# Performance work log

Hardware: AMD Instinct MI355X
Metric: run time of the kernel (lower is better)

Reference implementation:

```python
import jax, jax.numpy as jnp
import numpy as np

H, C = 4, 32
NT, NDAT, NDEV = 50000, 20000, 4
EDT, EVT, ETT = 800000, 200000, 400000


def _gat_conv(xs, xd, src, dst, ea, Ws, Wd, We, As, Ad, Ae, b, n_dst, concat):
    # linear projections -> [N, H, C]
    hs = (xs @ Ws).reshape(-1, H, C)
    hd = (xd @ Wd).reshape(-1, H, C)
    he = (ea @ We).reshape(-1, H, C)
    # per-edge attention logits [E, H]
    al = (hs * As).sum(-1)[src] + (hd * Ad).sum(-1)[dst] + (he * Ae).sum(-1)
    al = jax.nn.leaky_relu(al, 0.2)
    # segment softmax over incoming edges of each dst node
    amax = jax.ops.segment_max(al, dst, num_segments=n_dst)
    amax = jnp.where(jnp.isfinite(amax), amax, 0.0)
    ex = jnp.exp(al - amax[dst])
    den = jax.ops.segment_sum(ex, dst, num_segments=n_dst)
    w = ex / (den[dst] + 1e-16)
    # weighted scatter-add of source messages
    out = jax.ops.segment_sum(hs[src] * w[..., None], dst, num_segments=n_dst)
    out = out.reshape(n_dst, H * C) if concat else out.mean(axis=1)
    return out + b


def _add_self_loops_mean(src, dst, ea, n):
    # PyG add_self_loops(fill_value='mean'): loop edge_attr = mean of incoming edge_attr per node
    cnt = jax.ops.segment_sum(jnp.ones(dst.shape, ea.dtype), dst, num_segments=n)
    ea_mean = jax.ops.segment_sum(ea, dst, num_segments=n) / jnp.maximum(cnt, 1.0)[:, None]
    loops = jnp.arange(n, dtype=src.dtype)
    return (jnp.concatenate([src, loops]), jnp.concatenate([dst, loops]),
            jnp.concatenate([ea, ea_mean], axis=0))


def setup_inputs() -> dict:
    key = jax.random.key(0)
    ks = iter(jax.random.split(key, 40))
    nrm = lambda shape, fan: jax.random.normal(next(ks), shape, jnp.float32) / np.sqrt(fan)
    inp = {}
    inp['x_data'] = jax.random.normal(next(ks), (NDAT, 8), jnp.float32)
    inp['x_tasks'] = jax.random.normal(next(ks), (NT, 16), jnp.float32)
    inp['x_dev'] = jax.random.normal(next(ks), (NDEV, 8), jnp.float32)
    inp['ei_dt'] = jnp.stack([jax.random.randint(next(ks), (EDT,), 0, NDAT),
                              jax.random.randint(next(ks), (EDT,), 0, NT)]).astype(jnp.int32)
    inp['ea_dt'] = jax.random.normal(next(ks), (EDT, 8), jnp.float32)
    inp['ei_vt'] = jnp.stack([jax.random.randint(next(ks), (EVT,), 0, NDEV),
                              jax.random.randint(next(ks), (EVT,), 0, NT)]).astype(jnp.int32)
    inp['ea_vt'] = jax.random.normal(next(ks), (EVT, 6), jnp.float32)
    inp['ei_tt'] = jnp.stack([jax.random.randint(next(ks), (ETT,), 0, NT),
                              jax.random.randint(next(ks), (ETT,), 0, NT)]).astype(jnp.int32)
    inp['ea_tt'] = jax.random.normal(next(ks), (ETT, 4), jnp.float32)
    # conv1: (data -> tasks), concat=True
    inp['Ws1'] = nrm((8, H * C), 8); inp['Wd1'] = nrm((16, H * C), 16); inp['We1'] = nrm((8, H * C), 8)
    inp['As1'] = nrm((H, C), C); inp['Ad1'] = nrm((H, C), C); inp['Ae1'] = nrm((H, C), C)
    inp['b1'] = jnp.zeros((H * C,), jnp.float32)
    # conv2: (devices -> tasks), concat=True
    inp['Ws2'] = nrm((8, H * C), 8); inp['Wd2'] = nrm((16, H * C), 16); inp['We2'] = nrm((6, H * C), 6)
    inp['As2'] = nrm((H, C), C); inp['Ad2'] = nrm((H, C), C); inp['Ae2'] = nrm((H, C), C)
    inp['b2'] = jnp.zeros((H * C,), jnp.float32)
    # conv3: tasks -> tasks, single lin (256 -> H*C), concat=False, self loops
    inp['W3'] = nrm((2 * H * C, H * C), 2 * H * C); inp['We3'] = nrm((4, H * C), 4)
    inp['As3'] = nrm((H, C), C); inp['Ad3'] = nrm((H, C), C); inp['Ae3'] = nrm((H, C), C)
    inp['b3'] = jnp.zeros((C,), jnp.float32)
    return inp


def reference(x_data, x_tasks, x_dev, ei_dt, ea_dt, ei_vt, ea_vt, ei_tt, ea_tt,
              Ws1, Wd1, We1, As1, Ad1, Ae1, b1,
              Ws2, Wd2, We2, As2, Ad2, Ae2, b2,
              W3, We3, As3, Ad3, Ae3, b3):
    t_data = jax.nn.relu(_gat_conv(x_data, x_tasks, ei_dt[0], ei_dt[1], ea_dt,
                                   Ws1, Wd1, We1, As1, Ad1, Ae1, b1, NT, True))
    t_dev = jax.nn.relu(_gat_conv(x_dev, x_tasks, ei_vt[0], ei_vt[1], ea_vt,
                                  Ws2, Wd2, We2, As2, Ad2, Ae2, b2, NT, True))
    tasks = jnp.concatenate([t_data, t_dev], axis=1)  # [NT, 256]
    src, dst, ea = _add_self_loops_mean(ei_tt[0], ei_tt[1], ea_tt, NT)
    x = _gat_conv(tasks, tasks, src, dst, ea, W3, W3, We3, As3, Ad3, Ae3, b3, NT, False)
    x = jax.nn.relu(x)
    # dropout(p=0.5) is identity in eval mode
    return x
```

## Files before the change

### kernel.cpp

```cpp
#include <hip/hip_runtime.h>
#include <math.h>

static const int NT = 50000, NDAT = 20000, NDEV = 4;
static const int EDT = 800000, EVT = 200000, ETT = 400000;

static const int SCAN_TILE = 2048, SCAN_NB = 25;

static const int IN_A = NDAT * 128;
static const int IN_B = IN_A + NDAT * 4;
static const int IN_C = IN_B + NT * 4;
static const int IN_D = IN_C + NDEV * 128;
static const int IN_E = IN_D + NDEV * 4;
static const int IN_F = IN_E + 256 * 128;

static const size_t OFF_TASKS = 0;
static const size_t OFF_HS    = 12800000;
static const size_t OFF_RANK  = OFF_HS;
static const size_t OFF_HSB1  = OFF_HS + 1400000;
static const size_t OFF_WV1   = OFF_HS + 2680000;
static const size_t OFF_WV2   = 19200000;
static const size_t OFF_ESRC1 = 20000000;
static const size_t OFF_ESRC2 = 20800000;
static const size_t OFF_PERM3 = 21200000;
static const size_t OFF_DEG   = 23200000;
static const size_t OFF_RP    = 23350000;
static const size_t OFF_AS1   = 23500004;
static const size_t OFF_AD1   = 23580004;
static const size_t OFF_AD2   = 23780004;
static const size_t OFF_HS2   = 23980004;
static const size_t OFF_AS2   = 23980516;
static const size_t OFF_QS1   = 23980532;
static const size_t OFF_QD1   = 23980564;
static const size_t OFF_P1    = 23980628;
static const size_t OFF_QS2   = 23980660;
static const size_t OFF_QD2   = 23980692;
static const size_t OFF_P2    = 23980756;
static const size_t OFF_P3    = 23980780;
static const size_t OFF_BSUM  = 23980796;
static const size_t OFF_W3HT  = 23980924;
static const size_t OFF_W3LT  = 23997308;
static const size_t WS_TOTAL  = 24013692;

typedef short v8s __attribute__((ext_vector_type(8)));
typedef float v4f __attribute__((ext_vector_type(4)));

__device__ __forceinline__ float lrelu(float a) { return a > 0.f ? a : 0.2f * a; }
__device__ __forceinline__ unsigned short f2bf(float x) {
    unsigned int u = __float_as_uint(x);
    return (unsigned short)((u + 0x7FFFu + ((u >> 16) & 1u)) >> 16);
}
__device__ __forceinline__ float bf2f(unsigned short h) {
    return __uint_as_float(((unsigned int)h) << 16);
}
__device__ __forceinline__ void cvt_split(const float4& A, const float4& B, v8s& hi, v8s& lo) {
    union { unsigned short u[8]; v8s v; } H, L;
    float f[8] = {A.x, A.y, A.z, A.w, B.x, B.y, B.z, B.w};
    #pragma unroll
    for (int i = 0; i < 8; ++i) {
        unsigned short h = f2bf(f[i]);
        H.u[i] = h;
        L.u[i] = f2bf(f[i] - bf2f(h));
    }
    hi = H.v; lo = L.v;
}

__global__ void k_proj_small(const float* Ws1, const float* As1,
                             const float* Wd1, const float* Ad1,
                             const float* We1, const float* Ae1,
                             const float* Ws2, const float* As2,
                             const float* Wd2, const float* Ad2,
                             const float* We2, const float* Ae2,
                             const float* We3, const float* Ae3,
                             float* Qs1, float* Qd1, float* P1,
                             float* Qs2, float* Qd2, float* P2, float* P3) {
    int t = threadIdx.x;
    const float *W, *A; float* O; int u;
    if      (t < 32)  { W = Ws1; A = As1; O = Qs1; u = t; }
    else if (t < 96)  { W = Wd1; A = Ad1; O = Qd1; u = t - 32; }
    else if (t < 128) { W = We1; A = Ae1; O = P1;  u = t - 96; }
    else if (t < 160) { W = Ws2; A = As2; O = Qs2; u = t - 128; }
    else if (t < 224) { W = Wd2; A = Ad2; O = Qd2; u = t - 160; }
    else if (t < 248) { W = We2; A = Ae2; O = P2;  u = t - 224; }
    else if (t < 264) { W = We3; A = Ae3; O = P3;  u = t - 248; }
    else return;
    int k = u >> 2, h = u & 3;
    float acc = 0.f;
    for (int c = 0; c < 32; ++c) acc += W[k * 128 + h * 32 + c] * A[h * 32 + c];
    O[k * 4 + h] = acc;
}

__global__ __launch_bounds__(256) void k_inputs(const float* __restrict__ x_data,
                                                const float* __restrict__ Ws1,
                                                unsigned short* __restrict__ hsb1,
                                                const float* __restrict__ Qs1,
                                                float* __restrict__ as1,
                                                const float* __restrict__ x_tasks,
                                                const float* __restrict__ Qd1,
                                                const float* __restrict__ Qd2,
                                                float* __restrict__ ad1, float* __restrict__ ad2,
                                                const float* __restrict__ x_dev,
                                                const float* __restrict__ Ws2,
                                                float* __restrict__ hs2,
                                                const float* __restrict__ Qs2,
                                                float* __restrict__ as2,
                                                const float* __restrict__ W3,
                                                unsigned short* __restrict__ w3hT,
                                                unsigned short* __restrict__ w3lT) {
    int idx = blockIdx.x * blockDim.x + threadIdx.x;
    if (idx < IN_A) {
        int n = idx >> 7, j = idx & 127;
        float acc = 0.f;
        #pragma unroll
        for (int k = 0; k < 8; ++k) acc += x_data[n * 8 + k] * Ws1[k * 128 + j];
        hsb1[idx] = f2bf(acc);
    } else if (idx < IN_B) {
        int i = idx - IN_A;
        int n = i >> 2, h = i & 3;
        float acc = 0.f;
        #pragma unroll
        for (int k = 0; k < 8; ++k) acc += x_data[n * 8 + k] * Qs1[k * 4 + h];
        as1[i] = acc;
    } else if (idx < IN_C) {
        int i = idx - IN_B;
        int n = i >> 2, h = i & 3;
        float a = 0.f, b = 0.f;
        #pragma unroll
        for (int k = 0; k < 16; ++k) {
            float v = x_tasks[n * 16 + k];
            a += v * Qd1[k * 4 + h];
            b += v * Qd2[k * 4 + h];
        }
        ad1[i] = a; ad2[i] = b;
    } else if (idx < IN_D) {
        int i = idx - IN_C;
        int n = i >> 7, j = i & 127;
        float acc = 0.f;
        #pragma unroll
        for (int k = 0; k < 8; ++k) acc += x_dev[n * 8 + k] * Ws2[k * 128 + j];
        hs2[i] = acc;
    } else if (idx < IN_E) {
        int i = idx - IN_D;
        int n = i >> 2, h = i & 3;
        float acc = 0.f;
        #pragma unroll
        for (int k = 0; k < 8; ++k) acc += x_dev[n * 8 + k] * Qs2[k * 4 + h];
        as2[i] = acc;
    } else if (idx < IN_F) {
        int i = idx - IN_E;
        int k = i >> 7, n = i & 127;
        float x = W3[i];
        unsigned short h = f2bf(x);
        w3hT[n * 256 + k] = h;
        w3lT[n * 256 + k] = f2bf(x - bf2f(h));
    }
}

__global__ void k_hist(const int* __restrict__ dt, const int* __restrict__ vt,
                       const int* __restrict__ tt, int* __restrict__ deg,
                       int* __restrict__ rank) {
    int e = blockIdx.x * blockDim.x + threadIdx.x;
    if (e < EDT) rank[e] = atomicAdd(&deg[dt[EDT + e]], 1);
    else if (e < EDT + EVT) rank[e] = atomicAdd(&deg[NT + vt[EVT + (e - EDT)]], 1);
    else if (e < EDT + EVT + ETT) rank[e] = atomicAdd(&deg[2 * NT + tt[ETT + (e - EDT - EVT)]], 1);
}

__global__ __launch_bounds__(256) void k_scan_part(const int* __restrict__ deg,
                                                   int* __restrict__ bsum) {
    int b = blockIdx.x;
    int g = b / SCAN_NB, t = b % SCAN_NB;
    int base = t * SCAN_TILE + threadIdx.x * 8;
    const int* dg = deg + (size_t)g * NT;
    int s = 0;
    if (base + 8 <= NT) {
        int4 a = *reinterpret_cast<const int4*>(dg + base);
        int4 c = *reinterpret_cast<const int4*>(dg + base + 4);
        s = a.x + a.y + a.z + a.w + c.x + c.y + c.z + c.w;
    } else {
        for (int i = 0; i < 8; ++i) if (base + i < NT) s += dg[base + i];
    }
    __shared__ int red[256];
    red[threadIdx.x] = s;
    __syncthreads();
    for (int off = 128; off > 0; off >>= 1) {
        if (threadIdx.x < off) red[threadIdx.x] += red[threadIdx.x + off];
        __syncthreads();
    }
    if (threadIdx.x == 0) bsum[b] = red[0];
}

__global__ void k_scan_bsum(int* __restrict__ bsum, int* __restrict__ rp) {
    int lane = threadIdx.x;
    for (int g = 0; g < 3; ++g) {
        int v = (lane < SCAN_NB) ? bsum[g * SCAN_NB + lane] : 0;
        int inc = v;
        #pragma unroll
        for (int off = 1; off < 32; off <<= 1) {
            int o = __shfl_up(inc, off, 32);
            if ((lane & 31) >= off) inc += o;
        }
        if (lane < SCAN_NB) bsum[g * SCAN_NB + lane] = inc - v;
        if (lane == SCAN_NB - 1) rp[(size_t)g * (NT + 1) + NT] = inc;
    }
}

__global__ __launch_bounds__(256) void k_scan_final(const int* __restrict__ deg,
                                                    const int* __restrict__ bsum,
                                                    int* __restrict__ rp) {
    int b = blockIdx.x;
    int g = b / SCAN_NB, t = b % SCAN_NB;
    int tid = threadIdx.x;
    int base = t * SCAN_TILE + tid * 8;
    const int* dg = deg + (size_t)g * NT;
    int* rpg = rp + (size_t)g * (NT + 1);
    int v[8];
    int s = 0;
    if (base + 8 <= NT) {
        int4 a = *reinterpret_cast<const int4*>(dg + base);
        int4 c = *reinterpret_cast<const int4*>(dg + base + 4);
        v[0] = a.x; v[1] = a.y; v[2] = a.z; v[3] = a.w;
        v[4] = c.x; v[5] = c.y; v[6] = c.z; v[7] = c.w;
        s = v[0] + v[1] + v[2] + v[3] + v[4] + v[5] + v[6] + v[7];
    } else {
        #pragma unroll
        for (int i = 0; i < 8; ++i) {
            v[i] = (base + i < NT) ? dg[base + i] : 0;
            s += v[i];
        }
    }
    __shared__ int sums[256];
    sums[tid] = s;
    __syncthreads();
    for (int off = 1; off < 256; off <<= 1) {
        int x = (tid >= off) ? sums[tid - off] : 0;
        __syncthreads();
        sums[tid] += x;
        __syncthreads();
    }
    int run = bsum[b] + (tid ? sums[tid - 1] : 0);
    #pragma unroll
    for (int i = 0; i < 8; ++i) {
        int idx = base + i;
        if (idx < NT) { rpg[idx] = run; run += v[i]; }
    }
}

__global__ void k_permute_w(const int* __restrict__ dt, const int* __restrict__ vt,
                            const int* __restrict__ tt, const int* __restrict__ rank,
                            const int* __restrict__ rp,
                            const float* __restrict__ as1, const float* __restrict__ ad1,
                            const float* __restrict__ P1, const float* __restrict__ ea1,
                            const float* __restrict__ as2, const float* __restrict__ ad2,
                            const float* __restrict__ P2, const float* __restrict__ ea2,
                            int* __restrict__ esrc1, float* __restrict__ wv1,
                            int* __restrict__ esrc2, float* __restrict__ wv2,
                            int2* __restrict__ perm3) {
    int e = blockIdx.x * blockDim.x + threadIdx.x;
    if (e < EDT) {
        int s = dt[e], d = dt[EDT + e];
        int slot = rp[d] + rank[e];
        esrc1[slot] = s;
        float l[4];
        #pragma unroll
        for (int h = 0; h < 4; ++h) l[h] = as1[s * 4 + h] + ad1[d * 4 + h];
        float4 A = *reinterpret_cast<const float4*>(&ea1[(size_t)e * 8]);
        float4 B = *reinterpret_cast<const float4*>(&ea1[(size_t)e * 8 + 4]);
        float ev[8] = {A.x, A.y, A.z, A.w, B.x, B.y, B.z, B.w};
        #pragma unroll
        for (int k = 0; k < 8; ++k)
            #pragma unroll
            for (int h = 0; h < 4; ++h) l[h] += ev[k] * P1[k * 4 + h];
        float4 w4 = make_float4(expf(lrelu(l[0])), expf(lrelu(l[1])),
                                expf(lrelu(l[2])), expf(lrelu(l[3])));
        *reinterpret_cast<float4*>(&wv1[(size_t)slot * 4]) = w4;
    } else if (e < EDT + EVT) {
        int ee = e - EDT;
        int s = vt[ee], d = vt[EVT + ee];
        int slot = rp[(NT + 1) + d] + rank[e];
        esrc2[slot] = s;
        float l[4];
        #pragma unroll
        for (int h = 0; h < 4; ++h) l[h] = as2[s * 4 + h] + ad2[d * 4 + h];
        float2 a = *reinterpret_cast<const float2*>(&ea2[(size_t)ee * 6]);
        float2 b = *reinterpret_cast<const float2*>(&ea2[(size_t)ee * 6 + 2]);
        float2 c = *reinterpret_cast<const float2*>(&ea2[(size_t)ee * 6 + 4]);
        float ev[6] = {a.x, a.y, b.x, b.y, c.x, c.y};
        #pragma unroll
        for (int k = 0; k < 6; ++k)
            #pragma unroll
            for (int h = 0; h < 4; ++h) l[h] += ev[k] * P2[k * 4 + h];
        float4 w4 = make_float4(expf(lrelu(l[0])), expf(lrelu(l[1])),
                                expf(lrelu(l[2])), expf(lrelu(l[3])));
        *reinterpret_cast<float4*>(&wv2[(size_t)slot * 4]) = w4;
    } else if (e < EDT + EVT + ETT) {
        int ee = e - EDT - EVT;
        int d = tt[ETT + ee];
        perm3[rp[2 * (NT + 1) + d] + rank[e]] = make_int2(tt[ee], ee);
    }
}

__global__ __launch_bounds__(256) void k_gather_c1(const int* __restrict__ rp,
                                                   const int* __restrict__ esrc,
                                                   const float* __restrict__ wv,
                                                   const unsigned short* __restrict__ hsb,
                                                   const float* __restrict__ bias,
                                                   float* __restrict__ tasks) {
    int tid = threadIdx.x;
    int d = blockIdx.x * 8 + (tid >> 5);
    int lane = tid & 31;
    int h = lane >> 3;
    int c0 = (lane & 7) * 4;
    int i0 = rp[d], i1 = rp[d + 1];
    float a0 = 0.f, a1 = 0.f, a2 = 0.f, a3 = 0.f, den = 0.f;
    int i = i0;
    for (; i + 4 <= i1; i += 4) {
        int s0 = esrc[i], s1 = esrc[i + 1], s2 = esrc[i + 2], s3 = esrc[i + 3];
        float w0 = wv[(size_t)i * 4 + h];
        float w1 = wv[(size_t)(i + 1) * 4 + h];
        float w2 = wv[(size_t)(i + 2) * 4 + h];
        float w3 = wv[(size_t)(i + 3) * 4 + h];
        ushort4 m0 = *reinterpret_cast<const ushort4*>(&hsb[(size_t)s0 * 128 + h * 32 + c0]);
        ushort4 m1 = *reinterpret_cast<const ushort4*>(&hsb[(size_t)s1 * 128 + h * 32 + c0]);
        ushort4 m2 = *reinterpret_cast<const ushort4*>(&hsb[(size_t)s2 * 128 + h * 32 + c0]);
        ushort4 m3 = *reinterpret_cast<const ushort4*>(&hsb[(size_t)s3 * 128 + h * 32 + c0]);
        a0 += w0 * bf2f(m0.x) + w1 * bf2f(m1.x) + w2 * bf2f(m2.x) + w3 * bf2f(m3.x);
        a1 += w0 * bf2f(m0.y) + w1 * bf2f(m1.y) + w2 * bf2f(m2.y) + w3 * bf2f(m3.y);
        a2 += w0 * bf2f(m0.z) + w1 * bf2f(m1.z) + w2 * bf2f(m2.z) + w3 * bf2f(m3.z);
        a3 += w0 * bf2f(m0.w) + w1 * bf2f(m1.w) + w2 * bf2f(m2.w) + w3 * bf2f(m3.w);
        den += w0 + w1 + w2 + w3;
    }
    for (; i < i1; ++i) {
        int s = esrc[i];
        float w = wv[(size_t)i * 4 + h];
        ushort4 m = *reinterpret_cast<const ushort4*>(&hsb[(size_t)s * 128 + h * 32 + c0]);
        a0 += w * bf2f(m.x); a1 += w * bf2f(m.y);
        a2 += w * bf2f(m.z); a3 += w * bf2f(m.w);
        den += w;
    }
    int j0 = h * 32 + c0;
    float4 b4 = *reinterpret_cast<const float4*>(&bias[j0]);
    float r = 1.f / (den + 1e-16f);
    float4 o = make_float4(fmaxf(a0 * r + b4.x, 0.f), fmaxf(a1 * r + b4.y, 0.f),
                           fmaxf(a2 * r + b4.z, 0.f), fmaxf(a3 * r + b4.w, 0.f));
    *reinterpret_cast<float4*>(&tasks[(size_t)d * 256 + j0]) = o;
}

__global__ __launch_bounds__(256) void k_gather_c2(const int* __restrict__ rp,
                                                   const int* __restrict__ esrc,
                                                   const float* __restrict__ wv,
                                                   const float* __restrict__ hs2,
                                                   const float* __restrict__ bias,
                                                   float* __restrict__ tasks) {
    int tid = threadIdx.x;
    int d = blockIdx.x * 8 + (tid >> 5);
    int lane = tid & 31;
    int h = lane >> 3;
    int i0 = rp[d], i1 = rp[d + 1];
    float ax = 0.f, ay = 0.f, az = 0.f, aw = 0.f, den = 0.f;
    int i = i0;
    for (; i + 4 <= i1; i += 4) {
        int s0 = esrc[i], s1 = esrc[i + 1], s2 = esrc[i + 2], s3 = esrc[i + 3];
        float w0 = wv[(size_t)i * 4 + h];
        float w1 = wv[(size_t)(i + 1) * 4 + h];
        float w2 = wv[(size_t)(i + 2) * 4 + h];
        float w3 = wv[(size_t)(i + 3) * 4 + h];
        float4 v0 = *reinterpret_cast<const float4*>(&hs2[s0 * 128 + lane * 4]);
        float4 v1 = *reinterpret_cast<const float4*>(&hs2[s1 * 128 + lane * 4]);
        float4 v2 = *reinterpret_cast<const float4*>(&hs2[s2 * 128 + lane * 4]);
        float4 v3 = *reinterpret_cast<const float4*>(&hs2[s3 * 128 + lane * 4]);
        ax += v0.x * w0 + v1.x * w1 + v2.x * w2 + v3.x * w3;
        ay += v0.y * w0 + v1.y * w1 + v2.y * w2 + v3.y * w3;
        az += v0.z * w0 + v1.z * w1 + v2.z * w2 + v3.z * w3;
        aw += v0.w * w0 + v1.w * w1 + v2.w * w2 + v3.w * w3;
        den += w0 + w1 + w2 + w3;
    }
    for (; i < i1; ++i) {
        int s = esrc[i];
        float w = wv[(size_t)i * 4 + h];
        float4 v = *reinterpret_cast<const float4*>(&hs2[s * 128 + lane * 4]);
        ax += v.x * w; ay += v.y * w; az += v.z * w; aw += v.w * w;
        den += w;
    }
    float4 b4 = *reinterpret_cast<const float4*>(&bias[lane * 4]);
    float r = 1.f / (den + 1e-16f);
    float4 o = make_float4(fmaxf(ax * r + b4.x, 0.f), fmaxf(ay * r + b4.y, 0.f),
                           fmaxf(az * r + b4.z, 0.f), fmaxf(aw * r + b4.w, 0.f));
    *reinterpret_cast<float4*>(&tasks[(size_t)d * 256 + 128 + lane * 4]) = o;
}

__global__ void k_alpha_from_h2(const float* __restrict__ hs, const float* __restrict__ As,
                                const float* __restrict__ Ad, float* __restrict__ oa,
                                float* __restrict__ ob, unsigned short* __restrict__ hsb,
                                int N) {
    int idx = blockIdx.x * blockDim.x + threadIdx.x;
    if (idx >= N * 4) return;
    int n = idx >> 2, h = idx & 3;
    const float* row = hs + (size_t)n * 128 + h * 32;
    unsigned short* brow = hsb + (size_t)n * 128 + h * 32;
    float a = 0.f, b = 0.f;
    #pragma unroll
    for (int c = 0; c < 32; c += 4) {
        float4 v = *reinterpret_cast<const float4*>(row + c);
        a += v.x * As[h * 32 + c]     + v.y * As[h * 32 + c + 1]
           + v.z * As[h * 32 + c + 2] + v.w * As[h * 32 + c + 3];
        b += v.x * Ad[h * 32 + c]     + v.y * Ad[h * 32 + c + 1]
           + v.z * Ad[h * 32 + c + 2] + v.w * Ad[h * 32 + c + 3];
        ushort4 pk;
        pk.x = f2bf(v.x); pk.y = f2bf(v.y); pk.z = f2bf(v.z); pk.w = f2bf(v.w);
        *reinterpret_cast<ushort4*>(brow + c) = pk;
    }
    oa[idx] = a; ob[idx] = b;
}

__global__ __launch_bounds__(256) void k_gather_c3(const int* __restrict__ rp,
                                                   const int2* __restrict__ perm,
                                                   const float* __restrict__ as3,
                                                   const float* __restrict__ ad3,
                                                   const float* __restrict__ P3,
                                                   const float* __restrict__ ea,
                                                   const unsigned short* __restrict__ hsb,
                                                   const float* __restrict__ b3,
                                                   float* __restrict__ out) {
    int tid = threadIdx.x;
    int d = blockIdx.x * 8 + (tid >> 5);
    int lane = tid & 31;
    int h = lane >> 3;
    int c0 = (lane & 7) * 4;
    float Pk[4];
    #pragma unroll
    for (int k = 0; k < 4; ++k) Pk[k] = P3[k * 4 + h];
    float adv = ad3[d * 4 + h];
    int i0 = rp[d], i1 = rp[d + 1];
    float a0 = 0.f, a1 = 0.f, a2 = 0.f, a3 = 0.f, den = 0.f, aes = 0.f;
    int i = i0;
    for (; i + 4 <= i1; i += 4) {
        int2 p0 = perm[i], p1 = perm[i + 1], p2 = perm[i + 2], p3 = perm[i + 3];
        float s0 = as3[(size_t)p0.x * 4 + h], s1 = as3[(size_t)p1.x * 4 + h];
        float s2 = as3[(size_t)p2.x * 4 + h], s3 = as3[(size_t)p3.x * 4 + h];
        float4 q0 = *reinterpret_cast<const float4*>(&ea[(size_t)p0.y * 4]);
        float4 q1 = *reinterpret_cast<const float4*>(&ea[(size_t)p1.y * 4]);
        float4 q2 = *reinterpret_cast<const float4*>(&ea[(size_t)p2.y * 4]);
        float4 q3 = *reinterpret_cast<const float4*>(&ea[(size_t)p3.y * 4]);
        ushort4 m0 = *reinterpret_cast<const ushort4*>(&hsb[(size_t)p0.x * 128 + h * 32 + c0]);
        ushort4 m1 = *reinterpret_cast<const ushort4*>(&hsb[(size_t)p1.x * 128 + h * 32 + c0]);
        ushort4 m2 = *reinterpret_cast<const ushort4*>(&hsb[(size_t)p2.x * 128 + h * 32 + c0]);
        ushort4 m3 = *reinterpret_cast<const ushort4*>(&hsb[(size_t)p3.x * 128 + h * 32 + c0]);
        float ae0 = q0.x * Pk[0] + q0.y * Pk[1] + q0.z * Pk[2] + q0.w * Pk[3];
        float ae1 = q1.x * Pk[0] + q1.y * Pk[1] + q1.z * Pk[2] + q1.w * Pk[3];
        float ae2 = q2.x * Pk[0] + q2.y * Pk[1] + q2.z * Pk[2] + q2.w * Pk[3];
        float ae3 = q3.x * Pk[0] + q3.y * Pk[1] + q3.z * Pk[2] + q3.w * Pk[3];
        float w0 = expf(lrelu(s0 + adv + ae0));
        float w1 = expf(lrelu(s1 + adv + ae1));
        float w2 = expf(lrelu(s2 + adv + ae2));
        float w3 = expf(lrelu(s3 + adv + ae3));
        a0 += w0 * bf2f(m0.x) + w1 * bf2f(m1.x) + w2 * bf2f(m2.x) + w3 * bf2f(m3.x);
        a1 += w0 * bf2f(m0.y) + w1 * bf2f(m1.y) + w2 * bf2f(m2.y) + w3 * bf2f(m3.y);
        a2 += w0 * bf2f(m0.z) + w1 * bf2f(m1.z) + w2 * bf2f(m2.z) + w3 * bf2f(m3.z);
        a3 += w0 * bf2f(m0.w) + w1 * bf2f(m1.w) + w2 * bf2f(m2.w) + w3 * bf2f(m3.w);
        den += w0 + w1 + w2 + w3;
        aes += ae0 + ae1 + ae2 + ae3;
    }
    for (; i < i1; ++i) {
        int2 p = perm[i];
        float s = as3[(size_t)p.x * 4 + h];
        float4 q = *reinterpret_cast<const float4*>(&ea[(size_t)p.y * 4]);
        ushort4 m = *reinterpret_cast<const ushort4*>(&hsb[(size_t)p.x * 128 + h * 32 + c0]);
        float ae = q.x * Pk[0] + q.y * Pk[1] + q.z * Pk[2] + q.w * Pk[3];
        float w = expf(lrelu(s + adv + ae));
        a0 += w * bf2f(m.x); a1 += w * bf2f(m.y);
        a2 += w * bf2f(m.z); a3 += w * bf2f(m.w);
        den += w; aes += ae;
    }
    float cnt = (float)(i1 - i0);
    float mloop = aes / fmaxf(cnt, 1.f);
    float exl = expf(lrelu(as3[(size_t)d * 4 + h] + adv + mloop));
    ushort4 md = *reinterpret_cast<const ushort4*>(&hsb[(size_t)d * 128 + h * 32 + c0]);
    float rden = 1.f / (den + exl + 1e-16f);
    float p0 = (a0 + exl * bf2f(md.x)) * rden;
    float p1 = (a1 + exl * bf2f(md.y)) * rden;
    float p2 = (a2 + exl * bf2f(md.z)) * rden;
    float p3 = (a3 + exl * bf2f(md.w)) * rden;
    p0 += __shfl_xor(p0, 8, 32); p0 += __shfl_xor(p0, 16, 32);
    p1 += __shfl_xor(p1, 8, 32); p1 += __shfl_xor(p1, 16, 32);
    p2 += __shfl_xor(p2, 8, 32); p2 += __shfl_xor(p2, 16, 32);
    p3 += __shfl_xor(p3, 8, 32); p3 += __shfl_xor(p3, 16, 32);
    if ((lane >> 3) == 0) {
        float4 o;
        o.x = fmaxf(0.25f * p0 + b3[c0 + 0], 0.f);
        o.y = fmaxf(0.25f * p1 + b3[c0 + 1], 0.f);
        o.z = fmaxf(0.25f * p2 + b3[c0 + 2], 0.f);
        o.w = fmaxf(0.25f * p3 + b3[c0 + 3], 0.f);
        *reinterpret_cast<float4*>(&out[(size_t)d * 32 + c0]) = o;
    }
}

__global__ __launch_bounds__(256, 2) void k_gemm_mfma(const float* __restrict__ T,
                                                      const unsigned short* __restrict__ w3hT,
                                                      const unsigned short* __restrict__ w3lT,
                                                      float* __restrict__ outp) {
    __shared__ uint4 sB[2][2048];
    int tid = threadIdx.x;
    int lane = tid & 63;
    int wid = tid >> 6;
    int arow = lane & 15;
    int kgrp = lane >> 4;
    int s0 = blockIdx.x * 8 + wid * 2;
    int ss0 = s0 < 3125 ? s0 : 3124;
    int ss1 = (s0 + 1) < 3125 ? (s0 + 1) : 3124;
    const uint4* w3h4 = reinterpret_cast<const uint4*>(w3hT);
    const uint4* w3l4 = reinterpret_cast<const uint4*>(w3lT);

    v4f acc[2][8];
    #pragma unroll
    for (int sp = 0; sp < 2; ++sp)
        #pragma unroll
        for (int nt = 0; nt < 8; ++nt) acc[sp][nt] = (v4f)0.f;

    #pragma unroll
    for (int kt = 0; kt < 2; ++kt) {
        __syncthreads();
        float4 a0[8], a1[8];
        const float* Ta0 = T + (size_t)(ss0 * 16 + arow) * 256 + kt * 128 + kgrp * 8;
        const float* Ta1 = T + (size_t)(ss1 * 16 + arow) * 256 + kt * 128 + kgrp * 8;
        #pragma unroll
        for (int kc = 0; kc < 4; ++kc) {
            a0[kc * 2]     = *reinterpret_cast<const float4*>(Ta0 + kc * 32);
            a0[kc * 2 + 1] = *reinterpret_cast<const float4*>(Ta0 + kc * 32 + 4);
            a1[kc * 2]     = *reinterpret_cast<const float4*>(Ta1 + kc * 32);
            a1[kc * 2 + 1] = *reinterpret_cast<const float4*>(Ta1 + kc * 32 + 4);
        }
        #pragma unroll
        for (int it = 0; it < 8; ++it) {
            int c = it * 256 + tid;
            int n = c >> 4, ch = c & 15;
            int gi = n * 32 + kt * 16 + ch;
            int li = n * 16 + (ch ^ (n & 7));
            sB[0][li] = w3h4[gi];
            sB[1][li] = w3l4[gi];
        }
        __syncthreads();
        #pragma unroll
        for (int kc = 0; kc < 4; ++kc) {
            v8s ah0, al0, ah1, al1;
            cvt_split(a0[kc * 2], a0[kc * 2 + 1], ah0, al0);
            cvt_split(a1[kc * 2], a1[kc * 2 + 1], ah1, al1);
            #pragma unroll
            for (int nt = 0; nt < 8; ++nt) {
                int col = nt * 16 + arow;
                int ch = kc * 4 + kgrp;
                int li = col * 16 + (ch ^ (col & 7));
                v8s bh = *reinterpret_cast<const v8s*>(&sB[0][li]);
                v8s bl = *reinterpret_cast<const v8s*>(&sB[1][li]);
                acc[0][nt] = __builtin_amdgcn_mfma_f32_16x16x32_bf16(ah0, bh, acc[0][nt], 0, 0, 0);
                acc[0][nt] = __builtin_amdgcn_mfma_f32_16x16x32_bf16(ah0, bl, acc[0][nt], 0, 0, 0);
                acc[0][nt] = __builtin_amdgcn_mfma_f32_16x16x32_bf16(al0, bh, acc[0][nt], 0, 0, 0);
                acc[1][nt] = __builtin_amdgcn_mfma_f32_16x16x32_bf16(ah1, bh, acc[1][nt], 0, 0, 0);
                acc[1][nt] = __builtin_amdgcn_mfma_f32_16x16x32_bf16(ah1, bl, acc[1][nt], 0, 0, 0);
                acc[1][nt] = __builtin_amdgcn_mfma_f32_16x16x32_bf16(al1, bh, acc[1][nt], 0, 0, 0);
            }
        }
    }
    if (s0 < 3125) {
        #pragma unroll
        for (int nt = 0; nt < 8; ++nt)
            #pragma unroll
            for (int i = 0; i < 4; ++i)
                outp[(size_t)(s0 * 16 + kgrp * 4 + i) * 128 + nt * 16 + arow] = acc[0][nt][i];
    }
    if (s0 + 1 < 3125) {
        #pragma unroll
        for (int nt = 0; nt < 8; ++nt)
            #pragma unroll
            for (int i = 0; i < 4; ++i)
                outp[(size_t)((s0 + 1) * 16 + kgrp * 4 + i) * 128 + nt * 16 + arow] = acc[1][nt][i];
    }
}

extern "C" void kernel_launch(void* const* d_in, const int* in_sizes, int n_in,
                              void* d_out, int out_size, void* d_ws, size_t ws_size,
                              hipStream_t stream) {
    const float* x_data  = (const float*)d_in[0];
    const float* x_tasks = (const float*)d_in[1];
    const float* x_dev   = (const float*)d_in[2];
    const int*   ei_dt   = (const int*)d_in[3];
    const float* ea_dt   = (const float*)d_in[4];
    const int*   ei_vt   = (const int*)d_in[5];
    const float* ea_vt   = (const float*)d_in[6];
    const int*   ei_tt   = (const int*)d_in[7];
    const float* ea_tt   = (const float*)d_in[8];
    const float* Ws1 = (const float*)d_in[9];  const float* Wd1 = (const float*)d_in[10];
    const float* We1 = (const float*)d_in[11]; const float* As1 = (const float*)d_in[12];
    const float* Ad1 = (const float*)d_in[13]; const float* Ae1 = (const float*)d_in[14];
    const float* b1  = (const float*)d_in[15];
    const float* Ws2 = (const float*)d_in[16]; const float* Wd2 = (const float*)d_in[17];
    const float* We2 = (const float*)d_in[18]; const float* As2 = (const float*)d_in[19];
    const float* Ad2 = (const float*)d_in[20]; const float* Ae2 = (const float*)d_in[21];
    const float* b2  = (const float*)d_in[22];
    const float* W3  = (const float*)d_in[23]; const float* We3 = (const float*)d_in[24];
    const float* As3 = (const float*)d_in[25]; const float* Ad3 = (const float*)d_in[26];
    const float* Ae3 = (const float*)d_in[27]; const float* b3  = (const float*)d_in[28];

    if (ws_size < WS_TOTAL * sizeof(float)) return;

    float* w = (float*)d_ws;
    float* tasks = w + OFF_TASKS;
    unsigned short* hsb3 = (unsigned short*)(w + OFF_TASKS);
    float* hs    = w + OFF_HS;
    int*   rank  = (int*)(w + OFF_RANK);
    unsigned short* hsb1 = (unsigned short*)(w + OFF_HSB1);
    float* wv1   = w + OFF_WV1;
    float* wv2   = w + OFF_WV2;
    int*   esrc1 = (int*)(w + OFF_ESRC1);
    int*   esrc2 = (int*)(w + OFF_ESRC2);
    int2*  perm3 = (int2*)(w + OFF_PERM3);
    int*   deg   = (int*)(w + OFF_DEG);
    int*   rp    = (int*)(w + OFF_RP);
    int*   bsum  = (int*)(w + OFF_BSUM);
    unsigned short* w3hT = (unsigned short*)(w + OFF_W3HT);
    unsigned short* w3lT = (unsigned short*)(w + OFF_W3LT);
    float* as1 = w + OFF_AS1;
    float* ad1 = w + OFF_AD1; float* as3 = w + OFF_AD1;
    float* ad2 = w + OFF_AD2; float* ad3 = w + OFF_AD2;
    float* hs2 = w + OFF_HS2; float* as2 = w + OFF_AS2;
    float* Qs1 = w + OFF_QS1; float* Qd1 = w + OFF_QD1; float* P1 = w + OFF_P1;
    float* Qs2 = w + OFF_QS2; float* Qd2 = w + OFF_QD2; float* P2 = w + OFF_P2;
    float* P3  = w + OFF_P3;
    float* out = (float*)d_out;

    dim3 B(256);
    #define GRID(n) dim3((unsigned)(((n) + 255) / 256))

    hipMemsetAsync(deg, 0, 3 * NT * sizeof(int), stream);
    k_proj_small<<<1, 320, 0, stream>>>(Ws1, As1, Wd1, Ad1, We1, Ae1,
                                        Ws2, As2, Wd2, Ad2, We2, Ae2, We3, Ae3,
                                        Qs1, Qd1, P1, Qs2, Qd2, P2, P3);
    k_inputs<<<GRID(IN_F), B, 0, stream>>>(x_data, Ws1, hsb1, Qs1, as1,
                                           x_tasks, Qd1, Qd2, ad1, ad2,
                                           x_dev, Ws2, hs2, Qs2, as2,
                                           W3, w3hT, w3lT);
    k_hist<<<GRID(EDT + EVT + ETT), B, 0, stream>>>(ei_dt, ei_vt, ei_tt, deg, rank);
    k_scan_part<<<dim3(3 * SCAN_NB), B, 0, stream>>>(deg, bsum);
    k_scan_bsum<<<1, 64, 0, stream>>>(bsum, rp);
    k_scan_final<<<dim3(3 * SCAN_NB), B, 0, stream>>>(deg, bsum, rp);
    k_permute_w<<<GRID(EDT + EVT + ETT), B, 0, stream>>>(ei_dt, ei_vt, ei_tt, rank, rp,
                                                         as1, ad1, P1, ea_dt,
                                                         as2, ad2, P2, ea_vt,
                                                         esrc1, wv1, esrc2, wv2, perm3);
    k_gather_c1<<<dim3(NT / 8), B, 0, stream>>>(rp, esrc1, wv1, hsb1, b1, tasks);
    k_gather_c2<<<dim3(NT / 8), B, 0, stream>>>(rp + (NT + 1), esrc2, wv2, hs2, b2, tasks);

    k_gemm_mfma<<<dim3(391), dim3(256), 0, stream>>>(tasks, w3hT, w3lT, hs);
    k_alpha_from_h2<<<GRID(NT * 4), B, 0, stream>>>(hs, As3, Ad3, as3, ad3, hsb3, NT);
    k_gather_c3<<<dim3(NT / 8), B, 0, stream>>>(rp + 2 * (NT + 1), perm3, as3, ad3, P3, ea_tt,
                                                hsb3, b3, out);
    #undef GRID
}
```

Before: 243.5 us.

## Pack per-edge source and bf16 attention terms into 16-byte CSR records

The separate CSR arrays for source index and fp32 edge weights are replaced by one 16-byte record per edge, holding the source index and the four per-head exp-weights packed as bf16. For the third conv, the edge-attribute attention term is now computed in the permute kernel and stored in the record. This removes the random gather of edge attributes by original edge id in the last gather kernel. Each gather loads one record per edge instead of two streams, at the cost of bf16 rounding of weights and edge logits and one padding word per record.

```diff
diff --git a/kernel.cpp b/kernel.cpp
--- a/kernel.cpp
+++ b/kernel.cpp
@@ -17,11 +17,9 @@
 static const size_t OFF_HS    = 12800000;
 static const size_t OFF_RANK  = OFF_HS;
 static const size_t OFF_HSB1  = OFF_HS + 1400000;
-static const size_t OFF_WV1   = OFF_HS + 2680000;
-static const size_t OFF_WV2   = 19200000;
-static const size_t OFF_ESRC1 = 20000000;
-static const size_t OFF_ESRC2 = 20800000;
-static const size_t OFF_PERM3 = 21200000;
+static const size_t OFF_REC1  = OFF_HS + 2680000;
+static const size_t OFF_REC2  = 19200000;
+static const size_t OFF_REC3  = 20000000;
 static const size_t OFF_DEG   = 23200000;
 static const size_t OFF_RP    = 23350000;
 static const size_t OFF_AS1   = 23500004;
@@ -51,6 +49,10 @@
 }
 __device__ __forceinline__ float bf2f(unsigned short h) {
     return __uint_as_float(((unsigned int)h) << 16);
+}
+__device__ __forceinline__ float bfsel(unsigned int lo01, unsigned int lo23, int h) {
+    unsigned int word = (h < 2) ? lo01 : lo23;
+    return bf2f((unsigned short)((h & 1) ? (word >> 16) : (word & 0xFFFFu)));
 }
 __device__ __forceinline__ void cvt_split(const float4& A, const float4& B, v8s& hi, v8s& lo) {
     union { unsigned short u[8]; v8s v; } H, L;
@@ -251,14 +253,13 @@
                             const float* __restrict__ P1, const float* __restrict__ ea1,
                             const float* __restrict__ as2, const float* __restrict__ ad2,
                             const float* __restrict__ P2, const float* __restrict__ ea2,
-                            int* __restrict__ esrc1, float* __restrict__ wv1,
-                            int* __restrict__ esrc2, float* __restrict__ wv2,
-                            int2* __restrict__ perm3) {
+                            const float* __restrict__ P3, const float* __restrict__ ea3,
+                            uint4* __restrict__ rec1, uint4* __restrict__ rec2,
+                            uint4* __restrict__ rec3) {
     int e = blockIdx.x * blockDim.x + threadIdx.x;
     if (e < EDT) {
         int s = dt[e], d = dt[EDT + e];
         int slot = rp[d] + rank[e];
-        esrc1[slot] = s;
         float l[4];
         #pragma unroll
         for (int h = 0; h < 4; ++h) l[h] = as1[s * 4 + h] + ad1[d * 4 + h];
@@ -269,14 +270,15 @@
         for (int k = 0; k < 8; ++k)
             #pragma unroll
             for (int h = 0; h < 4; ++h) l[h] += ev[k] * P1[k * 4 + h];
-        float4 w4 = make_float4(expf(lrelu(l[0])), expf(lrelu(l[1])),
-                                expf(lrelu(l[2])), expf(lrelu(l[3])));
-        *reinterpret_cast<float4*>(&wv1[(size_t)slot * 4]) = w4;
+        unsigned int w01 = (unsigned int)f2bf(expf(lrelu(l[0])))
+                         | ((unsigned int)f2bf(expf(lrelu(l[1]))) << 16);
+        unsigned int w23 = (unsigned int)f2bf(expf(lrelu(l[2])))
+                         | ((unsigned int)f2bf(expf(lrelu(l[3]))) << 16);
+        rec1[slot] = make_uint4(w01, w23, (unsigned int)s, 0u);
     } else if (e < EDT + EVT) {
         int ee = e - EDT;
         int s = vt[ee], d = vt[EVT + ee];
         int slot = rp[(NT + 1) + d] + rank[e];
-        esrc2[slot] = s;
         float l[4];
         #pragma unroll
         for (int h = 0; h < 4; ++h) l[h] = as2[s * 4 + h] + ad2[d * 4 + h];
@@ -288,19 +290,28 @@
         for (int k = 0; k < 6; ++k)
             #pragma unroll
             for (int h = 0; h < 4; ++h) l[h] += ev[k] * P2[k * 4 + h];
-        float4 w4 = make_float4(expf(lrelu(l[0])), expf(lrelu(l[1])),
-                                expf(lrelu(l[2])), expf(lrelu(l[3])));
-        *reinterpret_cast<float4*>(&wv2[(size_t)slot * 4]) = w4;
+        unsigned int w01 = (unsigned int)f2bf(expf(lrelu(l[0])))
+                         | ((unsigned int)f2bf(expf(lrelu(l[1]))) << 16);
+        unsigned int w23 = (unsigned int)f2bf(expf(lrelu(l[2])))
+                         | ((unsigned int)f2bf(expf(lrelu(l[3]))) << 16);
+        rec2[slot] = make_uint4(w01, w23, (unsigned int)s, 0u);
     } else if (e < EDT + EVT + ETT) {
         int ee = e - EDT - EVT;
-        int d = tt[ETT + ee];
-        perm3[rp[2 * (NT + 1) + d] + rank[e]] = make_int2(tt[ee], ee);
+        int s = tt[ee], d = tt[ETT + ee];
+        int slot = rp[2 * (NT + 1) + d] + rank[e];
+        float4 q = *reinterpret_cast<const float4*>(&ea3[(size_t)ee * 4]);
+        float ae[4];
+        #pragma unroll
+        for (int h = 0; h < 4; ++h)
+            ae[h] = q.x * P3[h] + q.y * P3[4 + h] + q.z * P3[8 + h] + q.w * P3[12 + h];
+        unsigned int a01 = (unsigned int)f2bf(ae[0]) | ((unsigned int)f2bf(ae[1]) << 16);
+        unsigned int a23 = (unsigned int)f2bf(ae[2]) | ((unsigned int)f2bf(ae[3]) << 16);
+        rec3[slot] = make_uint4((unsigned int)s, a01, a23, 0u);
     }
 }
 
 __global__ __launch_bounds__(256) void k_gather_c1(const int* __restrict__ rp,
-                                                   const int* __restrict__ esrc,
-                                                   const float* __restrict__ wv,
+                                                   const uint4* __restrict__ rec,
                                                    const unsigned short* __restrict__ hsb,
                                                    const float* __restrict__ bias,
                                                    float* __restrict__ tasks) {
@@ -313,15 +324,15 @@
     float a0 = 0.f, a1 = 0.f, a2 = 0.f, a3 = 0.f, den = 0.f;
     int i = i0;
     for (; i + 4 <= i1; i += 4) {
-        int s0 = esrc[i], s1 = esrc[i + 1], s2 = esrc[i + 2], s3 = esrc[i + 3];
-        float w0 = wv[(size_t)i * 4 + h];
-        float w1 = wv[(size_t)(i + 1) * 4 + h];
-        float w2 = wv[(size_t)(i + 2) * 4 + h];
-        float w3 = wv[(size_t)(i + 3) * 4 + h];
-        ushort4 m0 = *reinterpret_cast<const ushort4*>(&hsb[(size_t)s0 * 128 + h * 32 + c0]);
-        ushort4 m1 = *reinterpret_cast<const ushort4*>(&hsb[(size_t)s1 * 128 + h * 32 + c0]);
-        ushort4 m2 = *reinterpret_cast<const ushort4*>(&hsb[(size_t)s2 * 128 + h * 32 + c0]);
-        ushort4 m3 = *reinterpret_cast<const ushort4*>(&hsb[(size_t)s3 * 128 + h * 32 + c0]);
+        uint4 r0 = rec[i], r1 = rec[i + 1], r2 = rec[i + 2], r3 = rec[i + 3];
+        float w0 = bfsel(r0.x, r0.y, h);
+        float w1 = bfsel(r1.x, r1.y, h);
+        float w2 = bfsel(r2.x, r2.y, h);
+        float w3 = bfsel(r3.x, r3.y, h);
+        ushort4 m0 = *reinterpret_cast<const ushort4*>(&hsb[(size_t)r0.z * 128 + h * 32 + c0]);
+        ushort4 m1 = *reinterpret_cast<const ushort4*>(&hsb[(size_t)r1.z * 128 + h * 32 + c0]);
+        ushort4 m2 = *reinterpret_cast<const ushort4*>(&hsb[(size_t)r2.z * 128 + h * 32 + c0]);
+        ushort4 m3 = *reinterpret_cast<const ushort4*>(&hsb[(size_t)r3.z * 128 + h * 32 + c0]);
         a0 += w0 * bf2f(m0.x) + w1 * bf2f(m1.x) + w2 * bf2f(m2.x) + w3 * bf2f(m3.x);
         a1 += w0 * bf2f(m0.y) + w1 * bf2f(m1.y) + w2 * bf2f(m2.y) + w3 * bf2f(m3.y);
         a2 += w0 * bf2f(m0.z) + w1 * bf2f(m1.z) + w2 * bf2f(m2.z) + w3 * bf2f(m3.z);
@@ -329,9 +340,9 @@
         den += w0 + w1 + w2 + w3;
     }
     for (; i < i1; ++i) {
-        int s = esrc[i];
-        float w = wv[(size_t)i * 4 + h];
-        ushort4 m = *reinterpret_cast<const ushort4*>(&hsb[(size_t)s * 128 + h * 32 + c0]);
+        uint4 r = rec[i];
+        float w = bfsel(r.x, r.y, h);
+        ushort4 m = *reinterpret_cast<const ushort4*>(&hsb[(size_t)r.z * 128 + h * 32 + c0]);
         a0 += w * bf2f(m.x); a1 += w * bf2f(m.y);
         a2 += w * bf2f(m.z); a3 += w * bf2f(m.w);
         den += w;
@@ -345,8 +356,7 @@
 }
 
 __global__ __launch_bounds__(256) void k_gather_c2(const int* __restrict__ rp,
-                                                   const int* __restrict__ esrc,
-                                                   const float* __restrict__ wv,
+                                                   const uint4* __restrict__ rec,
                                                    const float* __restrict__ hs2,
                                                    const float* __restrict__ bias,
                                                    float* __restrict__ tasks) {
@@ -358,15 +368,15 @@
     float ax = 0.f, ay = 0.f, az = 0.f, aw = 0.f, den = 0.f;
     int i = i0;
     for (; i + 4 <= i1; i += 4) {
-        int s0 = esrc[i], s1 = esrc[i + 1], s2 = esrc[i + 2], s3 = esrc[i + 3];
-        float w0 = wv[(size_t)i * 4 + h];
-        float w1 = wv[(size_t)(i + 1) * 4 + h];
-        float w2 = wv[(size_t)(i + 2) * 4 + h];
-        float w3 = wv[(size_t)(i + 3) * 4 + h];
-        float4 v0 = *reinterpret_cast<const float4*>(&hs2[s0 * 128 + lane * 4]);
-        float4 v1 = *reinterpret_cast<const float4*>(&hs2[s1 * 128 + lane * 4]);
-        float4 v2 = *reinterpret_cast<const float4*>(&hs2[s2 * 128 + lane * 4]);
-        float4 v3 = *reinterpret_cast<const float4*>(&hs2[s3 * 128 + lane * 4]);
+        uint4 r0 = rec[i], r1 = rec[i + 1], r2 = rec[i + 2], r3 = rec[i + 3];
+        float w0 = bfsel(r0.x, r0.y, h);
+        float w1 = bfsel(r1.x, r1.y, h);
+        float w2 = bfsel(r2.x, r2.y, h);
+        float w3 = bfsel(r3.x, r3.y, h);
+        float4 v0 = *reinterpret_cast<const float4*>(&hs2[r0.z * 128 + lane * 4]);
+        float4 v1 = *reinterpret_cast<const float4*>(&hs2[r1.z * 128 + lane * 4]);
+        float4 v2 = *reinterpret_cast<const float4*>(&hs2[r2.z * 128 + lane * 4]);
+        float4 v3 = *reinterpret_cast<const float4*>(&hs2[r3.z * 128 + lane * 4]);
         ax += v0.x * w0 + v1.x * w1 + v2.x * w2 + v3.x * w3;
         ay += v0.y * w0 + v1.y * w1 + v2.y * w2 + v3.y * w3;
         az += v0.z * w0 + v1.z * w1 + v2.z * w2 + v3.z * w3;
@@ -374,9 +384,9 @@
         den += w0 + w1 + w2 + w3;
     }
     for (; i < i1; ++i) {
-        int s = esrc[i];
-        float w = wv[(size_t)i * 4 + h];
-        float4 v = *reinterpret_cast<const float4*>(&hs2[s * 128 + lane * 4]);
+        uint4 r4 = rec[i];
+        float w = bfsel(r4.x, r4.y, h);
+        float4 v = *reinterpret_cast<const float4*>(&hs2[r4.z * 128 + lane * 4]);
         ax += v.x * w; ay += v.y * w; az += v.z * w; aw += v.w * w;
         den += w;
     }
@@ -412,11 +422,9 @@
 }
 
 __global__ __launch_bounds__(256) void k_gather_c3(const int* __restrict__ rp,
-                                                   const int2* __restrict__ perm,
+                                                   const uint4* __restrict__ rec,
                                                    const float* __restrict__ as3,
                                                    const float* __restrict__ ad3,
-                                                   const float* __restrict__ P3,
-                                                   const float* __restrict__ ea,
                                                    const unsigned short* __restrict__ hsb,
                                                    const float* __restrict__ b3,
                                                    float* __restrict__ out) {
@@ -425,29 +433,22 @@
     int lane = tid & 31;
     int h = lane >> 3;
     int c0 = (lane & 7) * 4;
-    float Pk[4];
-    #pragma unroll
-    for (int k = 0; k < 4; ++k) Pk[k] = P3[k * 4 + h];
     float adv = ad3[d * 4 + h];
     int i0 = rp[d], i1 = rp[d + 1];
     float a0 = 0.f, a1 = 0.f, a2 = 0.f, a3 = 0.f, den = 0.f, aes = 0.f;
     int i = i0;
     for (; i + 4 <= i1; i += 4) {
-        int2 p0 = perm[i], p1 = perm[i + 1], p2 = perm[i + 2], p3 = perm[i + 3];
-        float s0 = as3[(size_t)p0.x * 4 + h], s1 = as3[(size_t)p1.x * 4 + h];
-        float s2 = as3[(size_t)p2.x * 4 + h], s3 = as3[(size_t)p3.x * 4 + h];
-        float4 q0 = *reinterpret_cast<const float4*>(&ea[(size_t)p0.y * 4]);
-        float4 q1 = *reinterpret_cast<const float4*>(&ea[(size_t)p1.y * 4]);
-        float4 q2 = *reinterpret_cast<const float4*>(&ea[(size_t)p2.y * 4]);
-        float4 q3 = *reinterpret_cast<const float4*>(&ea[(size_t)p3.y * 4]);
-        ushort4 m0 = *reinterpret_cast<const ushort4*>(&hsb[(size_t)p0.x * 128 + h * 32 + c0]);
-        ushort4 m1 = *reinterpret_cast<const ushort4*>(&hsb[(size_t)p1.x * 128 + h * 32 + c0]);
-        ushort4 m2 = *reinterpret_cast<const ushort4*>(&hsb[(size_t)p2.x * 128 + h * 32 + c0]);
-        ushort4 m3 = *reinterpret_cast<const ushort4*>(&hsb[(size_t)p3.x * 128 + h * 32 + c0]);
-        float ae0 = q0.x * Pk[0] + q0.y * Pk[1] + q0.z * Pk[2] + q0.w * Pk[3];
-        float ae1 = q1.x * Pk[0] + q1.y * Pk[1] + q1.z * Pk[2] + q1.w * Pk[3];
-        float ae2 = q2.x * Pk[0] + q2.y * Pk[1] + q2.z * Pk[2] + q2.w * Pk[3];
-        float ae3 = q3.x * Pk[0] + q3.y * Pk[1] + q3.z * Pk[2] + q3.w * Pk[3];
+        uint4 r0 = rec[i], r1 = rec[i + 1], r2 = rec[i + 2], r3 = rec[i + 3];
+        float s0 = as3[(size_t)r0.x * 4 + h], s1 = as3[(size_t)r1.x * 4 + h];
+        float s2 = as3[(size_t)r2.x * 4 + h], s3 = as3[(size_t)r3.x * 4 + h];
+        ushort4 m0 = *reinterpret_cast<const ushort4*>(&hsb[(size_t)r0.x * 128 + h * 32 + c0]);
+        ushort4 m1 = *reinterpret_cast<const ushort4*>(&hsb[(size_t)r1.x * 128 + h * 32 + c0]);
+        ushort4 m2 = *reinterpret_cast<const ushort4*>(&hsb[(size_t)r2.x * 128 + h * 32 + c0]);
+        ushort4 m3 = *reinterpret_cast<const ushort4*>(&hsb[(size_t)r3.x * 128 + h * 32 + c0]);
+        float ae0 = bfsel(r0.y, r0.z, h);
+        float ae1 = bfsel(r1.y, r1.z, h);
+        float ae2 = bfsel(r2.y, r2.z, h);
+        float ae3 = bfsel(r3.y, r3.z, h);
         float w0 = expf(lrelu(s0 + adv + ae0));
         float w1 = expf(lrelu(s1 + adv + ae1));
         float w2 = expf(lrelu(s2 + adv + ae2));
@@ -460,11 +461,10 @@
         aes += ae0 + ae1 + ae2 + ae3;
     }
     for (; i < i1; ++i) {
-        int2 p = perm[i];
-        float s = as3[(size_t)p.x * 4 + h];
-        float4 q = *reinterpret_cast<const float4*>(&ea[(size_t)p.y * 4]);
-        ushort4 m = *reinterpret_cast<const ushort4*>(&hsb[(size_t)p.x * 128 + h * 32 + c0]);
-        float ae = q.x * Pk[0] + q.y * Pk[1] + q.z * Pk[2] + q.w * Pk[3];
+        uint4 r4 = rec[i];
+        float s = as3[(size_t)r4.x * 4 + h];
+        ushort4 m = *reinterpret_cast<const ushort4*>(&hsb[(size_t)r4.x * 128 + h * 32 + c0]);
+        float ae = bfsel(r4.y, r4.z, h);
         float w = expf(lrelu(s + adv + ae));
         a0 += w * bf2f(m.x); a1 += w * bf2f(m.y);
         a2 += w * bf2f(m.z); a3 += w * bf2f(m.w);
@@ -607,11 +607,9 @@
     float* hs    = w + OFF_HS;
     int*   rank  = (int*)(w + OFF_RANK);
     unsigned short* hsb1 = (unsigned short*)(w + OFF_HSB1);
-    float* wv1   = w + OFF_WV1;
-    float* wv2   = w + OFF_WV2;
-    int*   esrc1 = (int*)(w + OFF_ESRC1);
-    int*   esrc2 = (int*)(w + OFF_ESRC2);
-    int2*  perm3 = (int2*)(w + OFF_PERM3);
+    uint4* rec1  = (uint4*)(w + OFF_REC1);
+    uint4* rec2  = (uint4*)(w + OFF_REC2);
+    uint4* rec3  = (uint4*)(w + OFF_REC3);
     int*   deg   = (int*)(w + OFF_DEG);
     int*   rp    = (int*)(w + OFF_RP);
     int*   bsum  = (int*)(w + OFF_BSUM);
@@ -644,13 +642,14 @@
     k_permute_w<<<GRID(EDT + EVT + ETT), B, 0, stream>>>(ei_dt, ei_vt, ei_tt, rank, rp,
                                                          as1, ad1, P1, ea_dt,
                                                          as2, ad2, P2, ea_vt,
-                                                         esrc1, wv1, esrc2, wv2, perm3);
-    k_gather_c1<<<dim3(NT / 8), B, 0, stream>>>(rp, esrc1, wv1, hsb1, b1, tasks);
-    k_gather_c2<<<dim3(NT / 8), B, 0, stream>>>(rp + (NT + 1), esrc2, wv2, hs2, b2, tasks);
+                                                         P3, ea_tt,
+                                                         rec1, rec2, rec3);
+    k_gather_c1<<<dim3(NT / 8), B, 0, stream>>>(rp, rec1, hsb1, b1, tasks);
+    k_gather_c2<<<dim3(NT / 8), B, 0, stream>>>(rp + (NT + 1), rec2, hs2, b2, tasks);
 
     k_gemm_mfma<<<dim3(391), dim3(256), 0, stream>>>(tasks, w3hT, w3lT, hs);
     k_alpha_from_h2<<<GRID(NT * 4), B, 0, stream>>>(hs, As3, Ad3, as3, ad3, hsb3, NT);
-    k_gather_c3<<<dim3(NT / 8), B, 0, stream>>>(rp + 2 * (NT + 1), perm3, as3, ad3, P3, ea_tt,
+    k_gather_c3<<<dim3(NT / 8), B, 0, stream>>>(rp + 2 * (NT + 1), rec3, as3, ad3,
                                                 hsb3, b3, out);
     #undef GRID
 }
```

Measured after the change: 232.5 us. 4.5% less time.
